# Kernel optimization log

Hardware: AMD Instinct MI355X
Metric: run time of the kernel (lower is better)

Reference implementation:

```python
import jax, jax.numpy as jnp
import numpy as np

N = 100000
E = 1600000
NODE_IN = 8
EDGE_IN = 4
HID = 64
OUT = 4

# torch-initialized skip weights, in usage order (w2_1..w7_7)
SKIP_INIT = np.array([0.6, 0.4,
                      0.6, 0.4, 0.2,
                      0.6, 0.4, 0.2, 0.2,
                      0.6, 0.4, 0.2, 0.2, 0.2,
                      0.6, 0.4, 0.2, 0.2, 0.2, 0.2,
                      0.6, 0.4, 0.2, 0.2, 0.2, 0.2, 0.2], dtype=np.float32)

def _lin(key, fan_in, fan_out):
    b = 1.0 / np.sqrt(fan_in)
    k1, k2 = jax.random.split(key)
    W = jax.random.uniform(k1, (fan_in, fan_out), jnp.float32, -b, b)
    bias = jax.random.uniform(k2, (fan_out,), jnp.float32, -b, b)
    return W, bias

def setup_inputs() -> dict:
    key = jax.random.key(0)
    ks = jax.random.split(key, 20)
    x = jax.random.normal(ks[0], (N, NODE_IN), jnp.float32)
    edge_index = jax.random.randint(ks[1], (2, E), 0, N, jnp.int64)
    edge_attr = jax.random.normal(ks[2], (E, EDGE_IN), jnp.float32)
    # layer1
    Wm1, bm1 = _lin(ks[3], NODE_IN + EDGE_IN, HID)
    Wu1, bu1 = _lin(ks[4], NODE_IN + HID, HID)
    # mid layers (layers 2..6 of the torch module; layer7 is never used)
    Wm_mid, bm_mid, Wu_mid, bu_mid = [], [], [], []
    for i in range(5):
        Wm, bm = _lin(ks[5 + 2 * i], HID + EDGE_IN, HID)
        Wu, bu = _lin(ks[6 + 2 * i], HID + HID, HID)
        Wm_mid.append(Wm); bm_mid.append(bm); Wu_mid.append(Wu); bu_mid.append(bu)
    Wm_mid = jnp.stack(Wm_mid); bm_mid = jnp.stack(bm_mid)
    Wu_mid = jnp.stack(Wu_mid); bu_mid = jnp.stack(bu_mid)
    # last layer
    Wm_last, bm_last = _lin(ks[16], HID + EDGE_IN, OUT)
    Wu_last, bu_last = _lin(ks[17], HID + OUT, OUT)
    skip_weights = jnp.asarray(SKIP_INIT)
    return dict(x=x, edge_index=edge_index, edge_attr=edge_attr,
                Wm1=Wm1, bm1=bm1, Wu1=Wu1, bu1=bu1,
                Wm_mid=Wm_mid, bm_mid=bm_mid, Wu_mid=Wu_mid, bu_mid=bu_mid,
                Wm_last=Wm_last, bm_last=bm_last, Wu_last=Wu_last, bu_last=bu_last,
                skip_weights=skip_weights)

def _graph_layer(h, src, dst, edge_attr, Wm, bm, Wu, bu):
    # message: ReLU(Linear([h_src, e_attr]))  -> [E, out]
    m = jax.nn.relu(jnp.concatenate([h[src], edge_attr], axis=-1) @ Wm + bm)
    # sum-aggregate messages at destination nodes -> [N, out]
    agg = jax.ops.segment_sum(m, dst, num_segments=N)
    # node update: ReLU(Linear([h, agg]))
    return jax.nn.relu(jnp.concatenate([h, agg], axis=-1) @ Wu + bu)

def reference(x, edge_index, edge_attr,
              Wm1, bm1, Wu1, bu1,
              Wm_mid, bm_mid, Wu_mid, bu_mid,
              Wm_last, bm_last, Wu_last, bu_last,
              skip_weights):
    src, dst = edge_index[0], edge_index[1]
    sw = skip_weights
    L = lambda h, i: _graph_layer(h, src, dst, edge_attr,
                                  Wm_mid[i], bm_mid[i], Wu_mid[i], bu_mid[i])
    x1 = _graph_layer(x, src, dst, edge_attr, Wm1, bm1, Wu1, bu1)
    x2 = L(x1, 0)
    x2w = x1 * sw[0] + x2 * sw[1]
    x3 = L(x2w, 1)
    x3w = x1 * sw[2] + x2w * sw[3] + x3 * sw[4]
    x4 = L(x3w, 2)
    x4w = x1 * sw[5] + x2w * sw[6] + x3w * sw[7] + x4 * sw[8]
    x5 = L(x4w, 2)  # NOTE: source reuses layer4 here (faithful to bug)
    x5w = x1 * sw[9] + x2w * sw[10] + x3w * sw[11] + x4w * sw[12] + x5 * sw[13]
    x6 = L(x5w, 3)  # layer5
    x6w = x1 * sw[14] + x2w * sw[15] + x3w * sw[16] + x4w * sw[17] + x5w * sw[18] + x6 * sw[19]
    x7 = L(x6w, 4)  # layer6
    x7w = (x1 * sw[20] + x2w * sw[21] + x3w * sw[22] + x4w * sw[23]
           + x5w * sw[24] + x6w * sw[25] + x7 * sw[26])
    return _graph_layer(x7w, src, dst, edge_attr, Wm_last, bm_last, Wu_last, bu_last)
```

## Files before the change

kernel.cpp:

```cpp
#include <hip/hip_runtime.h>


#define WAVE 64

__global__ __launch_bounds__(256) void hist_kernel(
    const int* __restrict__ ei, int* __restrict__ cnt, int E)
{
    int t = blockIdx.x * blockDim.x + threadIdx.x;
    int nt = gridDim.x * blockDim.x;
    for (int e = t; e < E; e += nt) atomicAdd(&cnt[ei[E + e]], 1);
}

__global__ __launch_bounds__(256) void scan1_kernel(
    const int* __restrict__ cnt, int* __restrict__ out, int* __restrict__ bsum, int N)
{
    __shared__ int lds[256];
    int t = threadIdx.x;
    int base = blockIdx.x * 1024 + t * 4;
    int v0 = (base + 0 < N) ? cnt[base + 0] : 0;
    int v1 = (base + 1 < N) ? cnt[base + 1] : 0;
    int v2 = (base + 2 < N) ? cnt[base + 2] : 0;
    int v3 = (base + 3 < N) ? cnt[base + 3] : 0;
    int tsum = v0 + v1 + v2 + v3;
    lds[t] = tsum;
    __syncthreads();
    for (int off = 1; off < 256; off <<= 1) {
        int x = 0;
        if (t >= off) x = lds[t - off];
        __syncthreads();
        if (t >= off) lds[t] += x;
        __syncthreads();
    }
    int run = lds[t] - tsum;
    if (base + 0 < N) out[base + 0] = run; run += v0;
    if (base + 1 < N) out[base + 1] = run; run += v1;
    if (base + 2 < N) out[base + 2] = run; run += v2;
    if (base + 3 < N) out[base + 3] = run;
    if (t == 255) bsum[blockIdx.x] = lds[255];
}

__global__ __launch_bounds__(256) void scan2_kernel(int* __restrict__ bsum, int B)
{
    __shared__ int lds[256];
    __shared__ int carry;
    int t = threadIdx.x;
    if (t == 0) carry = 0;
    __syncthreads();
    for (int start = 0; start < B; start += 256) {
        int i = start + t;
        int v = (i < B) ? bsum[i] : 0;
        lds[t] = v;
        __syncthreads();
        for (int off = 1; off < 256; off <<= 1) {
            int x = 0;
            if (t >= off) x = lds[t - off];
            __syncthreads();
            if (t >= off) lds[t] += x;
            __syncthreads();
        }
        if (i < B) bsum[i] = carry + lds[t] - v;
        __syncthreads();
        if (t == 255) carry += lds[255];
        __syncthreads();
    }
}

__global__ __launch_bounds__(256) void scan3_kernel(
    int* __restrict__ rowptr, int* __restrict__ cursor,
    const int* __restrict__ bsum, int N, int E)
{
    int t = blockIdx.x * blockDim.x + threadIdx.x;
    int nt = gridDim.x * blockDim.x;
    for (int i = t; i < N; i += nt) {
        int v = rowptr[i] + bsum[i >> 10];
        rowptr[i] = v;
        cursor[i] = v;
    }
    if (t == 0) rowptr[N] = E;
}

__global__ __launch_bounds__(256) void scatter_kernel(
    const int* __restrict__ ei, const float* __restrict__ ea,
    int* __restrict__ cursor, int* __restrict__ srcp, float* __restrict__ eap, int E)
{
    int t = blockIdx.x * blockDim.x + threadIdx.x;
    int nt = gridDim.x * blockDim.x;
    for (int e = t; e < E; e += nt) {
        int d = ei[E + e];
        int pos = atomicAdd(&cursor[d], 1);
        srcp[pos] = ei[e];
        *reinterpret_cast<float4*>(eap + (size_t)4 * pos) =
            *reinterpret_cast<const float4*>(ea + (size_t)4 * e);
    }
}


template<int C>
__device__ __forceinline__ void stage_rows(
    const float* __restrict__ src, int rs, int base, int N, int t, float* As)
{
    constexpr int NFQ = C / 4;
    for (int idx = t; idx < 64 * NFQ; idx += 256) {
        int n = idx / NFQ, kq = idx % NFQ;
        int gn = min(base + n, N - 1);
        *reinterpret_cast<float4*>(As + n * 68 + 4 * kq) =
            *reinterpret_cast<const float4*>(src + (size_t)gn * rs + 4 * kq);
    }
}

template<int C>
__device__ __forceinline__ void stage_w(
    const float* __restrict__ Wg, int t, float* Ws)
{
    const float4* wsrc = reinterpret_cast<const float4*>(Wg);
    float4* wdst = reinterpret_cast<float4*>(Ws);
    for (int idx = t; idx < C * 16; idx += 256) wdst[idx] = wsrc[idx];
}

template<int C>
__device__ __forceinline__ void compute_rm(
    const float* As, const float* Ws, int tx, int ty, float acc[4][4])
{
#pragma unroll 2
    for (int k = 0; k < C; k += 4) {
        float4 w0 = *reinterpret_cast<const float4*>(Ws + (k + 0) * 64 + 4 * tx);
        float4 w1 = *reinterpret_cast<const float4*>(Ws + (k + 1) * 64 + 4 * tx);
        float4 w2 = *reinterpret_cast<const float4*>(Ws + (k + 2) * 64 + 4 * tx);
        float4 w3 = *reinterpret_cast<const float4*>(Ws + (k + 3) * 64 + 4 * tx);
#pragma unroll
        for (int i = 0; i < 4; ++i) {
            float4 a = *reinterpret_cast<const float4*>(As + (4 * ty + i) * 68 + k);
            acc[i][0] = fmaf(a.x, w0.x, acc[i][0]);
            acc[i][1] = fmaf(a.x, w0.y, acc[i][1]);
            acc[i][2] = fmaf(a.x, w0.z, acc[i][2]);
            acc[i][3] = fmaf(a.x, w0.w, acc[i][3]);
            acc[i][0] = fmaf(a.y, w1.x, acc[i][0]);
            acc[i][1] = fmaf(a.y, w1.y, acc[i][1]);
            acc[i][2] = fmaf(a.y, w1.z, acc[i][2]);
            acc[i][3] = fmaf(a.y, w1.w, acc[i][3]);
            acc[i][0] = fmaf(a.z, w2.x, acc[i][0]);
            acc[i][1] = fmaf(a.z, w2.y, acc[i][1]);
            acc[i][2] = fmaf(a.z, w2.z, acc[i][2]);
            acc[i][3] = fmaf(a.z, w2.w, acc[i][3]);
            acc[i][0] = fmaf(a.w, w3.x, acc[i][0]);
            acc[i][1] = fmaf(a.w, w3.y, acc[i][1]);
            acc[i][2] = fmaf(a.w, w3.z, acc[i][2]);
            acc[i][3] = fmaf(a.w, w3.w, acc[i][3]);
        }
    }
}

template<int K1, bool HASB, bool RELU, bool SKIPP, bool UPDP, bool INITP, bool HASP>
__global__ __launch_bounds__(256) void lin4_kernel(
    const float* __restrict__ A, const float* __restrict__ B,
    const float* __restrict__ W, const float* __restrict__ bias,
    float* __restrict__ out, float* __restrict__ P,
    const float* __restrict__ Wnext, const float* __restrict__ bnext,
    float* __restrict__ pout, int N,
    const float* __restrict__ sw, int csIdx, int ciIdx)
{
    __shared__ float As[64 * 68];
    __shared__ float Ws[64 * 64];
    int t = threadIdx.x;
    int tx = t & 15, ty = t >> 4;
    int base = blockIdx.x * 64;

    float acc[4][4];
    {
        float4 bv = *reinterpret_cast<const float4*>(bias + 4 * tx);
#pragma unroll
        for (int i = 0; i < 4; ++i) {
            acc[i][0] = bv.x; acc[i][1] = bv.y; acc[i][2] = bv.z; acc[i][3] = bv.w;
        }
    }

    stage_rows<K1>(A, K1, base, N, t, As);
    stage_w<K1>(W, t, Ws);
    __syncthreads();
    compute_rm<K1>(As, Ws, tx, ty, acc);

    if constexpr (HASB) {
        __syncthreads();
        stage_rows<64>(B, 64, base, N, t, As);
        stage_w<64>(W + (size_t)K1 * 64, t, Ws);
        __syncthreads();
        compute_rm<64>(As, Ws, tx, ty, acc);
    }

    float cs = 0.0f, ci = 0.0f;
    if (SKIPP) cs = sw[csIdx];
    if (UPDP || INITP) ci = sw[ciIdx];

    if constexpr (HASP) __syncthreads();

#pragma unroll
    for (int i = 0; i < 4; ++i) {
        int gn = base + 4 * ty + i;
        float r0 = acc[i][0], r1 = acc[i][1], r2 = acc[i][2], r3 = acc[i][3];
        if (RELU) {
            r0 = fmaxf(r0, 0.0f); r1 = fmaxf(r1, 0.0f);
            r2 = fmaxf(r2, 0.0f); r3 = fmaxf(r3, 0.0f);
        }
        size_t off = (size_t)gn * 64 + 4 * tx;
        float4 Pv = {0, 0, 0, 0};
        if (SKIPP && gn < N) {
            Pv = *reinterpret_cast<const float4*>(P + off);
            r0 = fmaf(cs, r0, Pv.x);
            r1 = fmaf(cs, r1, Pv.y);
            r2 = fmaf(cs, r2, Pv.z);
            r3 = fmaf(cs, r3, Pv.w);
        }
        if (gn < N) {
            float4 r; r.x = r0; r.y = r1; r.z = r2; r.w = r3;
            *reinterpret_cast<float4*>(out + off) = r;
            if (UPDP) {
                float4 Pn;
                Pn.x = fmaf(ci, r0, Pv.x);
                Pn.y = fmaf(ci, r1, Pv.y);
                Pn.z = fmaf(ci, r2, Pv.z);
                Pn.w = fmaf(ci, r3, Pv.w);
                *reinterpret_cast<float4*>(P + off) = Pn;
            }
            if (INITP) {
                float4 Pn;
                Pn.x = ci * r0; Pn.y = ci * r1; Pn.z = ci * r2; Pn.w = ci * r3;
                *reinterpret_cast<float4*>(P + off) = Pn;
            }
        }
        if (HASP) {
            float* as = As + (4 * ty + i) * 68 + 4 * tx;
            as[0] = r0; as[1] = r1; as[2] = r2; as[3] = r3;
        }
    }

    if constexpr (HASP) {
        stage_w<64>(Wnext, t, Ws);
        __syncthreads();
        float acc2[4][4];
        {
            float4 bv = *reinterpret_cast<const float4*>(bnext + 4 * tx);
#pragma unroll
            for (int i = 0; i < 4; ++i) {
                acc2[i][0] = bv.x; acc2[i][1] = bv.y; acc2[i][2] = bv.z; acc2[i][3] = bv.w;
            }
        }
        compute_rm<64>(As, Ws, tx, ty, acc2);
#pragma unroll
        for (int i = 0; i < 4; ++i) {
            int gn = base + 4 * ty + i;
            if (gn < N) {
                float4 r; r.x = acc2[i][0]; r.y = acc2[i][1]; r.z = acc2[i][2]; r.w = acc2[i][3];
                *reinterpret_cast<float4*>(pout + (size_t)gn * 64 + 4 * tx) = r;
            }
        }
    }
}

__global__ __launch_bounds__(256) void csr_agg_kernel(
    const int* __restrict__ rowptr, const int* __restrict__ srcp,
    const float* __restrict__ eap, const float* __restrict__ p,
    const float* __restrict__ Wme, float* __restrict__ agg, int N)
{
    int lane = threadIdx.x & 63;
    int g = lane >> 4;
    int q = lane & 15;
    int gwave = blockIdx.x * (blockDim.x >> 6) + (threadIdx.x >> 6);
    int nw = gridDim.x * (blockDim.x >> 6);
    float4 w0 = *reinterpret_cast<const float4*>(Wme + 0 * 64 + 4 * q);
    float4 w1 = *reinterpret_cast<const float4*>(Wme + 1 * 64 + 4 * q);
    float4 w2 = *reinterpret_cast<const float4*>(Wme + 2 * 64 + 4 * q);
    float4 w3 = *reinterpret_cast<const float4*>(Wme + 3 * 64 + 4 * q);

    for (int n = gwave; n < N; n += nw) {
        int beg = rowptr[n], end = rowptr[n + 1];
        int deg = end - beg;
        int nc = (deg + 3) >> 2;
        float4 acc = {0, 0, 0, 0};
        int sA = 0, sB = 0;
        float4 aA = {0, 0, 0, 0}, aB = {0, 0, 0, 0};
        bool vA = (g < deg);
        bool vB = (4 + g < deg);
        if (vA) { sA = srcp[beg + g];     aA = *reinterpret_cast<const float4*>(eap + (size_t)4 * (beg + g)); }
        if (vB) { sB = srcp[beg + 4 + g]; aB = *reinterpret_cast<const float4*>(eap + (size_t)4 * (beg + 4 + g)); }
        float4 pA = *reinterpret_cast<const float4*>(p + (size_t)sA * 64 + 4 * q);
        for (int c = 0; c < nc; ++c) {
            int sC = 0; float4 aC = {0, 0, 0, 0};
            bool vC = (4 * (c + 2) + g) < deg;
            if (vC) {
                int jc = beg + 4 * (c + 2) + g;
                sC = srcp[jc];
                aC = *reinterpret_cast<const float4*>(eap + (size_t)4 * jc);
            }
            float4 pB = *reinterpret_cast<const float4*>(p + (size_t)sB * 64 + 4 * q);
            float4 m;
            m.x = fmaf(aA.x, w0.x, fmaf(aA.y, w1.x, fmaf(aA.z, w2.x, fmaf(aA.w, w3.x, pA.x))));
            m.y = fmaf(aA.x, w0.y, fmaf(aA.y, w1.y, fmaf(aA.z, w2.y, fmaf(aA.w, w3.y, pA.y))));
            m.z = fmaf(aA.x, w0.z, fmaf(aA.y, w1.z, fmaf(aA.z, w2.z, fmaf(aA.w, w3.z, pA.z))));
            m.w = fmaf(aA.x, w0.w, fmaf(aA.y, w1.w, fmaf(aA.z, w2.w, fmaf(aA.w, w3.w, pA.w))));
            float f = vA ? 1.0f : 0.0f;
            acc.x = fmaf(f, fmaxf(m.x, 0.0f), acc.x);
            acc.y = fmaf(f, fmaxf(m.y, 0.0f), acc.y);
            acc.z = fmaf(f, fmaxf(m.z, 0.0f), acc.z);
            acc.w = fmaf(f, fmaxf(m.w, 0.0f), acc.w);
            vA = vB; aA = aB; pA = pB;
            vB = vC; aB = aC; sB = sC;
        }
        acc.x += __shfl_xor(acc.x, 16); acc.y += __shfl_xor(acc.y, 16);
        acc.z += __shfl_xor(acc.z, 16); acc.w += __shfl_xor(acc.w, 16);
        acc.x += __shfl_xor(acc.x, 32); acc.y += __shfl_xor(acc.y, 32);
        acc.z += __shfl_xor(acc.z, 32); acc.w += __shfl_xor(acc.w, 32);
        if (g == 0)
            *reinterpret_cast<float4*>(agg + (size_t)n * 64 + 4 * q) = acc;
    }
}

__global__ __launch_bounds__(256) void edge_kernel(
    const int* __restrict__ ei, const float* __restrict__ ea,
    const float* __restrict__ p, const float* __restrict__ Wme,
    float* __restrict__ agg, int E)
{
    int lane = threadIdx.x & 63;
    int gwave = blockIdx.x * (blockDim.x >> 6) + (threadIdx.x >> 6);
    int nw = gridDim.x * (blockDim.x >> 6);
    float w0 = Wme[0 * 64 + lane];
    float w1 = Wme[1 * 64 + lane];
    float w2 = Wme[2 * 64 + lane];
    float w3 = Wme[3 * 64 + lane];
    for (int e = gwave; e < E; e += nw) {
        int s = ei[e];
        int d = ei[E + e];
        float4 a = *reinterpret_cast<const float4*>(ea + (size_t)4 * e);
        float v = p[(size_t)s * 64 + lane];
        v = fmaf(a.x, w0, v);
        v = fmaf(a.y, w1, v);
        v = fmaf(a.z, w2, v);
        v = fmaf(a.w, w3, v);
        v = fmaxf(v, 0.0f);
        atomicAdd(agg + (size_t)d * 64 + lane, v);
    }
}

__global__ __launch_bounds__(256) void pl_kernel(
    const float* __restrict__ A, const float* __restrict__ W,
    const float* __restrict__ bias, float* __restrict__ out, int N)
{
    __shared__ float Wl[64 * 4];
    __shared__ float bl[4];
    for (int i = threadIdx.x; i < 256; i += blockDim.x) Wl[i] = W[i];
    if (threadIdx.x < 4) bl[threadIdx.x] = bias[threadIdx.x];
    __syncthreads();
    int t = blockIdx.x * blockDim.x + threadIdx.x;
    int nt = gridDim.x * blockDim.x;
    for (int idx = t; idx < N * 4; idx += nt) {
        int n = idx >> 2, f = idx & 3;
        float acc = bl[f];
        const float* ar = A + (size_t)n * 64;
#pragma unroll 4
        for (int kk = 0; kk < 16; ++kk) {
            float4 a4 = *reinterpret_cast<const float4*>(ar + 4 * kk);
            acc = fmaf(a4.x, Wl[(4 * kk + 0) * 4 + f], acc);
            acc = fmaf(a4.y, Wl[(4 * kk + 1) * 4 + f], acc);
            acc = fmaf(a4.z, Wl[(4 * kk + 2) * 4 + f], acc);
            acc = fmaf(a4.w, Wl[(4 * kk + 3) * 4 + f], acc);
        }
        out[idx] = acc;
    }
}

__global__ __launch_bounds__(256) void csr_agg4_kernel(
    const int* __restrict__ rowptr, const int* __restrict__ srcp,
    const float* __restrict__ eap, const float* __restrict__ p4,
    const float* __restrict__ Wme, float* __restrict__ agg4, int N)
{
    float w[16];
#pragma unroll
    for (int i = 0; i < 16; ++i) w[i] = Wme[i];
    int t = blockIdx.x * blockDim.x + threadIdx.x;
    int nt = gridDim.x * blockDim.x;
    for (int n = t; n < N; n += nt) {
        int beg = rowptr[n], end = rowptr[n + 1];
        float4 acc = {0, 0, 0, 0};
        for (int j = beg; j < end; ++j) {
            int s = srcp[j];
            float4 a = *reinterpret_cast<const float4*>(eap + (size_t)4 * j);
            float4 pv = *reinterpret_cast<const float4*>(p4 + (size_t)4 * s);
            float vx = pv.x + a.x * w[0] + a.y * w[4] + a.z * w[8]  + a.w * w[12];
            float vy = pv.y + a.x * w[1] + a.y * w[5] + a.z * w[9]  + a.w * w[13];
            float vz = pv.z + a.x * w[2] + a.y * w[6] + a.z * w[10] + a.w * w[14];
            float vw = pv.w + a.x * w[3] + a.y * w[7] + a.z * w[11] + a.w * w[15];
            acc.x += fmaxf(vx, 0.0f);
            acc.y += fmaxf(vy, 0.0f);
            acc.z += fmaxf(vz, 0.0f);
            acc.w += fmaxf(vw, 0.0f);
        }
        *reinterpret_cast<float4*>(agg4 + (size_t)4 * n) = acc;
    }
}

__global__ __launch_bounds__(256) void edge4_kernel(
    const int* __restrict__ ei, const float* __restrict__ ea,
    const float* __restrict__ p4, const float* __restrict__ Wme,
    float* __restrict__ agg4, int E)
{
    int lane = threadIdx.x & 63;
    int f = lane & 3;
    int gwave = blockIdx.x * (blockDim.x >> 6) + (threadIdx.x >> 6);
    int nw = gridDim.x * (blockDim.x >> 6);
    float w0 = Wme[0 * 4 + f];
    float w1 = Wme[1 * 4 + f];
    float w2 = Wme[2 * 4 + f];
    float w3 = Wme[3 * 4 + f];
    for (int e0 = gwave * 16; e0 < E; e0 += nw * 16) {
        int e = e0 + (lane >> 2);
        if (e < E) {
            int s = ei[e];
            int d = ei[E + e];
            float4 a = *reinterpret_cast<const float4*>(ea + (size_t)4 * e);
            float v = p4[(size_t)s * 4 + f];
            v = fmaf(a.x, w0, v);
            v = fmaf(a.y, w1, v);
            v = fmaf(a.z, w2, v);
            v = fmaf(a.w, w3, v);
            v = fmaxf(v, 0.0f);
            atomicAdd(agg4 + (size_t)d * 4 + f, v);
        }
    }
}

__global__ __launch_bounds__(256) void ul_kernel(
    const float* __restrict__ A, const float* __restrict__ agg4,
    const float* __restrict__ W , const float* __restrict__ bias,
    float* __restrict__ out, int N)
{
    __shared__ float Wl[68 * 4];
    __shared__ float bl[4];
    for (int i = threadIdx.x; i < 68 * 4; i += blockDim.x) Wl[i] = W[i];
    if (threadIdx.x < 4) bl[threadIdx.x] = bias[threadIdx.x];
    __syncthreads();
    int t = blockIdx.x * blockDim.x + threadIdx.x;
    int nt = gridDim.x * blockDim.x;
    for (int idx = t; idx < N * 4; idx += nt) {
        int n = idx >> 2, f = idx & 3;
        float acc = bl[f];
        const float* ar = A + (size_t)n * 64;
#pragma unroll 4
        for (int kk = 0; kk < 16; ++kk) {
            float4 a4 = *reinterpret_cast<const float4*>(ar + 4 * kk);
            acc = fmaf(a4.x, Wl[(4 * kk + 0) * 4 + f], acc);
            acc = fmaf(a4.y, Wl[(4 * kk + 1) * 4 + f], acc);
            acc = fmaf(a4.z, Wl[(4 * kk + 2) * 4 + f], acc);
            acc = fmaf(a4.w, Wl[(4 * kk + 3) * 4 + f], acc);
        }
        float4 g = *reinterpret_cast<const float4*>(agg4 + (size_t)n * 4);
        acc = fmaf(g.x, Wl[(64 + 0) * 4 + f], acc);
        acc = fmaf(g.y, Wl[(64 + 1) * 4 + f], acc);
        acc = fmaf(g.z, Wl[(64 + 2) * 4 + f], acc);
        acc = fmaf(g.w, Wl[(64 + 3) * 4 + f], acc);
        out[idx] = fmaxf(acc, 0.0f);
    }
}

extern "C" void kernel_launch(void* const* d_in, const int* in_sizes, int n_in,
                              void* d_out, int out_size, void* d_ws, size_t ws_size,
                              hipStream_t stream)
{
    const float* x      = (const float*)d_in[0];
    const int*   ei     = (const int*)d_in[1];
    const float* ea     = (const float*)d_in[2];
    const float* Wm1    = (const float*)d_in[3];
    const float* bm1    = (const float*)d_in[4];
    const float* Wu1    = (const float*)d_in[5];
    const float* bu1    = (const float*)d_in[6];
    const float* Wm_mid = (const float*)d_in[7];
    const float* bm_mid = (const float*)d_in[8];
    const float* Wu_mid = (const float*)d_in[9];
    const float* bu_mid = (const float*)d_in[10];
    const float* WmL    = (const float*)d_in[11];
    const float* bmL    = (const float*)d_in[12];
    const float* WuL    = (const float*)d_in[13];
    const float* buL    = (const float*)d_in[14];
    const float* sw     = (const float*)d_in[15];

    const int N = in_sizes[0] / 8;
    const int E = in_sizes[2] / 4;

    float* ws = (float*)d_ws;
    size_t nh = (size_t)N * 64;
    float* p    = ws;
    float* agg  = ws + nh;
    float* xwA  = ws + 2 * nh;
    float* xwB  = ws + 3 * nh;
    float* P    = ws + 4 * nh;
    float* p4   = agg;
    float* agg4 = agg + (size_t)N * 4;

    float* eap   = ws + 5 * nh;
    int*   srcp  = (int*)(eap + (size_t)E * 4);
    int*   rowptr= srcp + E;
    int*   cursor= rowptr + N + 1;
    int*   bsum  = cursor + N;
    size_t need_bytes = (5 * nh + (size_t)E * 4) * 4 + ((size_t)E + 2 * N + 1 + 1024) * 4;
    bool use_csr = ws_size >= need_bytes;

    dim3 blk(256);
    dim3 gEdge(2048), g4(1024);
    dim3 gLin((N + 63) / 64);
    const float* nul = nullptr;

    if (use_csr) {
        int B = (N + 1023) / 1024;
        hipMemsetAsync(cursor, 0, (size_t)N * 4, stream);
        hist_kernel<<<gEdge, blk, 0, stream>>>(ei, cursor, E);
        scan1_kernel<<<dim3(B), blk, 0, stream>>>(cursor, rowptr, bsum, N);
        scan2_kernel<<<dim3(1), blk, 0, stream>>>(bsum, B);
        scan3_kernel<<<dim3(256), blk, 0, stream>>>(rowptr, cursor, bsum, N, E);
        scatter_kernel<<<gEdge, blk, 0, stream>>>(ei, ea, cursor, srcp, eap, E);
    }

    auto edge_pass = [&](const float* pp, const float* Wme, float* aggout) {
        if (use_csr) {
            csr_agg_kernel<<<gEdge, blk, 0, stream>>>(rowptr, srcp, eap, pp, Wme, aggout, N);
        } else {
            hipMemsetAsync(aggout, 0, nh * sizeof(float), stream);
            edge_kernel<<<gEdge, blk, 0, stream>>>(ei, ea, pp, Wme, aggout, E);
        }
    };

    struct MidStep { int mi; const float* in; float* out; int cs; int ci; };
    MidStep steps[6] = {
        {0, xwA, xwB, 1,  3},
        {1, xwB, xwA, 4,  7},
        {2, xwA, xwB, 8,  12},
        {2, xwB, xwA, 13, 18},
        {3, xwA, xwB, 19, 25},
        {4, xwB, xwA, 26, 0},
    };

    lin4_kernel<8, false, false, false, false, false, false><<<gLin, blk, 0, stream>>>(
        x, nul, Wm1, bm1, p, nullptr, nul, nul, nullptr, N, sw, 0, 0);
    edge_pass(p, Wm1 + 8 * 64, agg);
    lin4_kernel<8, true, true, false, false, true, true><<<gLin, blk, 0, stream>>>(
        x, agg, Wu1, bu1, xwA, P,
        Wm_mid + (size_t)0 * 68 * 64, bm_mid + (size_t)0 * 64, p, N, sw, 0, 0);

    for (int li = 0; li < 6; ++li) {
        const MidStep& st = steps[li];
        const float* Wm = Wm_mid + (size_t)st.mi * 68 * 64;
        const float* Wu = Wu_mid + (size_t)st.mi * 128 * 64;
        const float* bu = bu_mid + (size_t)st.mi * 64;
        edge_pass(p, Wm + 64 * 64, agg);
        if (li < 5) {
            int nmi = steps[li + 1].mi;
            lin4_kernel<64, true, true, true, true, false, true><<<gLin, blk, 0, stream>>>(
                st.in, agg, Wu, bu, st.out, P,
                Wm_mid + (size_t)nmi * 68 * 64, bm_mid + (size_t)nmi * 64, p, N,
                sw, st.cs, st.ci);
        } else {
            lin4_kernel<64, true, true, true, false, false, false><<<gLin, blk, 0, stream>>>(
                st.in, agg, Wu, bu, st.out, P,
                nul, nul, nullptr, N, sw, st.cs, 0);
        }
    }
    float* x7w = steps[5].out;

    pl_kernel<<<g4, blk, 0, stream>>>(x7w, WmL, bmL, p4, N);
    if (use_csr) {
        csr_agg4_kernel<<<g4, blk, 0, stream>>>(rowptr, srcp, eap, p4, WmL + 64 * 4, agg4, N);
    } else {
        hipMemsetAsync(agg4, 0, (size_t)N * 4 * sizeof(float), stream);
        edge4_kernel<<<gEdge, blk, 0, stream>>>(ei, ea, p4, WmL + 64 * 4, agg4, E);
    }
    ul_kernel<<<g4, blk, 0, stream>>>(x7w, agg4, WuL, buL, (float*)d_out, N);
}
```

Before: 969.6 us.

## Store projected node features in bf16 for edge gathers; unroll CSR scatter

The per-node projection p, which every edge gather reads, is now written in bf16 by the linear kernels and widened back to fp32 inside the CSR aggregation and atomic edge kernels. This halves the bytes moved by the dominant random-gather traffic in each layer's edge pass. The CSR scatter kernel is also unrolled to handle four edges per thread so more loads and atomics are in flight. The cost is precision: messages are computed from rounded features, so accuracy drifts slightly from the fp32 reference.

Result: faster. 871.9 us (-10.1%).

```diff
diff --git a/kernel.cpp b/kernel.cpp
--- a/kernel.cpp
+++ b/kernel.cpp
@@ -2,6 +2,15 @@
 
 
 #define WAVE 64
+
+__device__ __forceinline__ unsigned short f2bf(float f) {
+    unsigned b = __float_as_uint(f);
+    unsigned r = b + 0x7FFFu + ((b >> 16) & 1u);
+    return (unsigned short)(r >> 16);
+}
+__device__ __forceinline__ float bf2f(unsigned short u) {
+    return __uint_as_float(((unsigned)u) << 16);
+}
 
 __global__ __launch_bounds__(256) void hist_kernel(
     const int* __restrict__ ei, int* __restrict__ cnt, int E)
@@ -85,12 +94,30 @@
 {
     int t = blockIdx.x * blockDim.x + threadIdx.x;
     int nt = gridDim.x * blockDim.x;
-    for (int e = t; e < E; e += nt) {
-        int d = ei[E + e];
-        int pos = atomicAdd(&cursor[d], 1);
-        srcp[pos] = ei[e];
-        *reinterpret_cast<float4*>(eap + (size_t)4 * pos) =
-            *reinterpret_cast<const float4*>(ea + (size_t)4 * e);
+    for (int eb = t; eb < E; eb += 4 * nt) {
+        int e0 = eb, e1 = eb + nt, e2 = eb + 2 * nt, e3 = eb + 3 * nt;
+        bool w1 = e1 < E, w2 = e2 < E, w3 = e3 < E;
+        int d0 = ei[E + e0];
+        int d1 = w1 ? ei[E + e1] : 0;
+        int d2 = w2 ? ei[E + e2] : 0;
+        int d3 = w3 ? ei[E + e3] : 0;
+        int s0 = ei[e0];
+        int s1 = w1 ? ei[e1] : 0;
+        int s2 = w2 ? ei[e2] : 0;
+        int s3 = w3 ? ei[e3] : 0;
+        float4 a0 = *reinterpret_cast<const float4*>(ea + (size_t)4 * e0);
+        float4 a1 = w1 ? *reinterpret_cast<const float4*>(ea + (size_t)4 * e1) : make_float4(0, 0, 0, 0);
+        float4 a2 = w2 ? *reinterpret_cast<const float4*>(ea + (size_t)4 * e2) : make_float4(0, 0, 0, 0);
+        float4 a3 = w3 ? *reinterpret_cast<const float4*>(ea + (size_t)4 * e3) : make_float4(0, 0, 0, 0);
+        int p0 = atomicAdd(&cursor[d0], 1);
+        int p1 = w1 ? atomicAdd(&cursor[d1], 1) : 0;
+        int p2 = w2 ? atomicAdd(&cursor[d2], 1) : 0;
+        int p3 = w3 ? atomicAdd(&cursor[d3], 1) : 0;
+        srcp[p0] = s0;
+        *reinterpret_cast<float4*>(eap + (size_t)4 * p0) = a0;
+        if (w1) { srcp[p1] = s1; *reinterpret_cast<float4*>(eap + (size_t)4 * p1) = a1; }
+        if (w2) { srcp[p2] = s2; *reinterpret_cast<float4*>(eap + (size_t)4 * p2) = a2; }
+        if (w3) { srcp[p3] = s3; *reinterpret_cast<float4*>(eap + (size_t)4 * p3) = a3; }
     }
 }
 
@@ -150,7 +177,7 @@
     }
 }
 
-template<int K1, bool HASB, bool RELU, bool SKIPP, bool UPDP, bool INITP, bool HASP>
+template<int K1, bool HASB, bool RELU, bool SKIPP, bool UPDP, bool INITP, bool HASP, bool OUTBF>
 __global__ __launch_bounds__(256) void lin4_kernel(
     const float* __restrict__ A, const float* __restrict__ B,
     const float* __restrict__ W, const float* __restrict__ bias,
@@ -211,8 +238,14 @@
             r3 = fmaf(cs, r3, Pv.w);
         }
         if (gn < N) {
-            float4 r; r.x = r0; r.y = r1; r.z = r2; r.w = r3;
-            *reinterpret_cast<float4*>(out + off) = r;
+            if (OUTBF) {
+                ushort4 u;
+                u.x = f2bf(r0); u.y = f2bf(r1); u.z = f2bf(r2); u.w = f2bf(r3);
+                *reinterpret_cast<ushort4*>(reinterpret_cast<unsigned short*>(out) + off) = u;
+            } else {
+                float4 r; r.x = r0; r.y = r1; r.z = r2; r.w = r3;
+                *reinterpret_cast<float4*>(out + off) = r;
+            }
             if (UPDP) {
                 float4 Pn;
                 Pn.x = fmaf(ci, r0, Pv.x);
@@ -249,8 +282,11 @@
         for (int i = 0; i < 4; ++i) {
             int gn = base + 4 * ty + i;
             if (gn < N) {
-                float4 r; r.x = acc2[i][0]; r.y = acc2[i][1]; r.z = acc2[i][2]; r.w = acc2[i][3];
-                *reinterpret_cast<float4*>(pout + (size_t)gn * 64 + 4 * tx) = r;
+                ushort4 u;
+                u.x = f2bf(acc2[i][0]); u.y = f2bf(acc2[i][1]);
+                u.z = f2bf(acc2[i][2]); u.w = f2bf(acc2[i][3]);
+                *reinterpret_cast<ushort4*>(
+                    reinterpret_cast<unsigned short*>(pout) + (size_t)gn * 64 + 4 * tx) = u;
             }
         }
     }
@@ -258,7 +294,7 @@
 
 __global__ __launch_bounds__(256) void csr_agg_kernel(
     const int* __restrict__ rowptr, const int* __restrict__ srcp,
-    const float* __restrict__ eap, const float* __restrict__ p,
+    const float* __restrict__ eap, const unsigned short* __restrict__ pb,
     const float* __restrict__ Wme, float* __restrict__ agg, int N)
 {
     int lane = threadIdx.x & 63;
@@ -282,7 +318,7 @@
         bool vB = (4 + g < deg);
         if (vA) { sA = srcp[beg + g];     aA = *reinterpret_cast<const float4*>(eap + (size_t)4 * (beg + g)); }
         if (vB) { sB = srcp[beg + 4 + g]; aB = *reinterpret_cast<const float4*>(eap + (size_t)4 * (beg + 4 + g)); }
-        float4 pA = *reinterpret_cast<const float4*>(p + (size_t)sA * 64 + 4 * q);
+        ushort4 pA = *reinterpret_cast<const ushort4*>(pb + (size_t)sA * 64 + 4 * q);
         for (int c = 0; c < nc; ++c) {
             int sC = 0; float4 aC = {0, 0, 0, 0};
             bool vC = (4 * (c + 2) + g) < deg;
@@ -291,12 +327,12 @@
                 sC = srcp[jc];
                 aC = *reinterpret_cast<const float4*>(eap + (size_t)4 * jc);
             }
-            float4 pB = *reinterpret_cast<const float4*>(p + (size_t)sB * 64 + 4 * q);
+            ushort4 pB = *reinterpret_cast<const ushort4*>(pb + (size_t)sB * 64 + 4 * q);
             float4 m;
-            m.x = fmaf(aA.x, w0.x, fmaf(aA.y, w1.x, fmaf(aA.z, w2.x, fmaf(aA.w, w3.x, pA.x))));
-            m.y = fmaf(aA.x, w0.y, fmaf(aA.y, w1.y, fmaf(aA.z, w2.y, fmaf(aA.w, w3.y, pA.y))));
-            m.z = fmaf(aA.x, w0.z, fmaf(aA.y, w1.z, fmaf(aA.z, w2.z, fmaf(aA.w, w3.z, pA.z))));
-            m.w = fmaf(aA.x, w0.w, fmaf(aA.y, w1.w, fmaf(aA.z, w2.w, fmaf(aA.w, w3.w, pA.w))));
+            m.x = fmaf(aA.x, w0.x, fmaf(aA.y, w1.x, fmaf(aA.z, w2.x, fmaf(aA.w, w3.x, bf2f(pA.x)))));
+            m.y = fmaf(aA.x, w0.y, fmaf(aA.y, w1.y, fmaf(aA.z, w2.y, fmaf(aA.w, w3.y, bf2f(pA.y)))));
+            m.z = fmaf(aA.x, w0.z, fmaf(aA.y, w1.z, fmaf(aA.z, w2.z, fmaf(aA.w, w3.z, bf2f(pA.z)))));
+            m.w = fmaf(aA.x, w0.w, fmaf(aA.y, w1.w, fmaf(aA.z, w2.w, fmaf(aA.w, w3.w, bf2f(pA.w)))));
             float f = vA ? 1.0f : 0.0f;
             acc.x = fmaf(f, fmaxf(m.x, 0.0f), acc.x);
             acc.y = fmaf(f, fmaxf(m.y, 0.0f), acc.y);
@@ -316,7 +352,7 @@
 
 __global__ __launch_bounds__(256) void edge_kernel(
     const int* __restrict__ ei, const float* __restrict__ ea,
-    const float* __restrict__ p, const float* __restrict__ Wme,
+    const unsigned short* __restrict__ pb, const float* __restrict__ Wme,
     float* __restrict__ agg, int E)
 {
     int lane = threadIdx.x & 63;
@@ -330,7 +366,7 @@
         int s = ei[e];
         int d = ei[E + e];
         float4 a = *reinterpret_cast<const float4*>(ea + (size_t)4 * e);
-        float v = p[(size_t)s * 64 + lane];
+        float v = bf2f(pb[(size_t)s * 64 + lane]);
         v = fmaf(a.x, w0, v);
         v = fmaf(a.y, w1, v);
         v = fmaf(a.z, w2, v);
@@ -519,10 +555,12 @@
 
     auto edge_pass = [&](const float* pp, const float* Wme, float* aggout) {
         if (use_csr) {
-            csr_agg_kernel<<<gEdge, blk, 0, stream>>>(rowptr, srcp, eap, pp, Wme, aggout, N);
+            csr_agg_kernel<<<gEdge, blk, 0, stream>>>(
+                rowptr, srcp, eap, (const unsigned short*)pp, Wme, aggout, N);
         } else {
             hipMemsetAsync(aggout, 0, nh * sizeof(float), stream);
-            edge_kernel<<<gEdge, blk, 0, stream>>>(ei, ea, pp, Wme, aggout, E);
+            edge_kernel<<<gEdge, blk, 0, stream>>>(
+                ei, ea, (const unsigned short*)pp, Wme, aggout, E);
         }
     };
 
@@ -536,10 +574,10 @@
         {4, xwB, xwA, 26, 0},
     };
 
-    lin4_kernel<8, false, false, false, false, false, false><<<gLin, blk, 0, stream>>>(
+    lin4_kernel<8, false, false, false, false, false, false, true><<<gLin, blk, 0, stream>>>(
         x, nul, Wm1, bm1, p, nullptr, nul, nul, nullptr, N, sw, 0, 0);
     edge_pass(p, Wm1 + 8 * 64, agg);
-    lin4_kernel<8, true, true, false, false, true, true><<<gLin, blk, 0, stream>>>(
+    lin4_kernel<8, true, true, false, false, true, true, false><<<gLin, blk, 0, stream>>>(
         x, agg, Wu1, bu1, xwA, P,
         Wm_mid + (size_t)0 * 68 * 64, bm_mid + (size_t)0 * 64, p, N, sw, 0, 0);
 
@@ -551,12 +589,12 @@
         edge_pass(p, Wm + 64 * 64, agg);
         if (li < 5) {
             int nmi = steps[li + 1].mi;
-            lin4_kernel<64, true, true, true, true, false, true><<<gLin, blk, 0, stream>>>(
+            lin4_kernel<64, true, true, true, true, false, true, false><<<gLin, blk, 0, stream>>>(
                 st.in, agg, Wu, bu, st.out, P,
                 Wm_mid + (size_t)nmi * 68 * 64, bm_mid + (size_t)nmi * 64, p, N,
                 sw, st.cs, st.ci);
         } else {
-            lin4_kernel<64, true, true, true, false, false, false><<<gLin, blk, 0, stream>>>(
+            lin4_kernel<64, true, true, true, false, false, false, false><<<gLin, blk, 0, stream>>>(
                 st.in, agg, Wu, bu, st.out, P,
                 nul, nul, nullptr, N, sw, st.cs, 0);
         }
```
